# Performance work log

Measured on AMD Instinct MI355X. Metric: run time of the kernel, lower is better.

The kernel has to match this reference:

```python
import jax, jax.numpy as jnp
import numpy as np
import math

MODULE_NUM = 256
OUTPUT_DIM = 257
HID = 64          # self.hidden_dim
STEP_DIM = 16
BATCH = 1024
SOS = MODULE_NUM + 1
EOS = MODULE_NUM
MAX_LEN = MODULE_NUM


def setup_inputs() -> dict:
    key = jax.random.key(0)
    ks = jax.random.split(key, 12)
    s = 0.05
    f32 = jnp.float32
    return {
        "step": 100,
        "batch_size": BATCH,
        "token_embed": jax.random.normal(ks[0], (MODULE_NUM + 2, HID), f32) * s,
        "step_table": jax.random.normal(ks[1], (MAX_LEN + 1, STEP_DIM), f32) * s,
        "w_ih_f": jax.random.normal(ks[2], (3 * HID, HID), f32) * s,
        "w_hh_f": jax.random.normal(ks[3], (3 * HID, HID), f32) * s,
        "b_ih_f": jax.random.normal(ks[4], (3 * HID,), f32) * s,
        "b_hh_f": jax.random.normal(ks[5], (3 * HID,), f32) * s,
        "w_ih_b": jax.random.normal(ks[6], (3 * HID, HID), f32) * s,
        "w_hh_b": jax.random.normal(ks[7], (3 * HID, HID), f32) * s,
        "b_ih_b": jax.random.normal(ks[8], (3 * HID,), f32) * s,
        "b_hh_b": jax.random.normal(ks[9], (3 * HID,), f32) * s,
        "film_w": jax.random.normal(ks[10], (4 * HID, STEP_DIM), f32) * s,
        "film_b": jnp.zeros((4 * HID,), f32),
        "dec_w": jax.random.normal(ks[11], (OUTPUT_DIM, 2 * HID), f32) * s,
        "dec_b": jnp.zeros((OUTPUT_DIM,), f32),
    }


def _gru_cell(x, h, w_ih, w_hh, b_ih, b_hh):
    # PyTorch GRU cell math
    gi = x @ w_ih.T + b_ih              # [B, 3H]
    gh = h @ w_hh.T + b_hh              # [B, 3H]
    i_r, i_z, i_n = jnp.split(gi, 3, axis=-1)
    h_r, h_z, h_n = jnp.split(gh, 3, axis=-1)
    r = jax.nn.sigmoid(i_r + h_r)
    z = jax.nn.sigmoid(i_z + h_z)
    n = jnp.tanh(i_n + r * h_n)
    return (1.0 - z) * n + z * h


def reference(step, batch_size, token_embed, step_table,
              w_ih_f, w_hh_f, b_ih_f, b_hh_f,
              w_ih_b, w_hh_b, b_ih_b, b_hh_b,
              film_w, film_b, dec_w, dec_b):
    # exponential-decay temperature (host scalar, matches _exp_decay_tau)
    tau_max, tau_min, half_life = 2.5, 0.2, 3000
    decay = math.log(2.0) / max(1, half_life)
    temperature = max(1e-06, tau_min + (tau_max - tau_min) * math.exp(-decay * max(0, int(step))))
    B = int(batch_size)

    def step_fn(carry, t):
        h_f, h_b, inp, sel, done = carry
        x = token_embed[inp]                              # [B, H]
        h_f2 = _gru_cell(x, h_f, w_ih_f, w_hh_f, b_ih_f, b_hh_f)
        h_b2 = _gru_cell(x, h_b, w_ih_b, w_hh_b, b_ih_b, b_hh_b)
        hs = jnp.concatenate([h_f2, h_b2], axis=-1)       # [B, 2H]
        film = jnp.tanh(step_table[t] @ film_w.T + film_b)  # [4H]
        gamma, beta = jnp.split(film, 2)
        hs = hs * (1.0 + gamma) + beta
        logits = hs @ dec_w.T + dec_b                     # [B, V]
        masked = jnp.where(sel, -jnp.inf, logits) / temperature
        logp = jax.nn.log_softmax(masked, axis=-1)
        action = jnp.argmax(logp, axis=-1)                # greedy (is_val=True)
        lp = jnp.take_along_axis(logp, action[:, None], axis=-1)[:, 0]
        valid = ~done
        done2 = done | (action == EOS)
        sel2 = sel.at[jnp.arange(B), action].set(True)
        return (h_f2, h_b2, action.astype(jnp.int32), sel2, done2), (action.astype(jnp.int32), lp * valid, valid)

    init = (jnp.zeros((B, HID), jnp.float32),
            jnp.zeros((B, HID), jnp.float32),
            jnp.full((B,), SOS, jnp.int32),
            jnp.zeros((B, OUTPUT_DIM), bool),
            jnp.zeros((B,), bool))
    _, (actions, log_probs, valid) = jax.lax.scan(step_fn, init, jnp.arange(MAX_LEN))
    # [B, L] layout; positions after EOS are masked out via `valid`
    return actions.T, log_probs.T, valid.T
```

## Files before the change

kernel.cpp:

```cpp
#include <hip/hip_runtime.h>
#include <cmath>

typedef float v2f __attribute__((ext_vector_type(2)));

#define GI_STRIDE (258*192)
#define FILM_OFF  (2*GI_STRIDE)
#define TOTAL_PRE (FILM_OFF + 256*256)

#define B_TOT   1024
#define L_MAX   256
#define SOS_TOK 257
#define EOS_TOK 256

#define KEEPF(x) asm volatile("" : "+v"(x))

#define PK_LO(acc, w, x) asm("v_pk_fma_f32 %0, %1, %2, %0 op_sel:[0,0,0] op_sel_hi:[1,0,1]" : "+v"(acc) : "v"(w), "v"(x))
#define PK_HI(acc, w, x) asm("v_pk_fma_f32 %0, %1, %2, %0 op_sel:[0,1,0] op_sel_hi:[1,1,1]" : "+v"(acc) : "v"(w), "v"(x))

#define DPPI(old, src, ctrl, rmask) __builtin_amdgcn_update_dpp(old, src, ctrl, rmask, 0xF, false)

#define AMAX_STAGE(ctrl, rmask) do { \
    const int   _vi = __builtin_bit_cast(int, mv); \
    const float _ov = __builtin_bit_cast(float, DPPI(_vi, _vi, ctrl, rmask)); \
    const int   _oi = DPPI(mi, mi, ctrl, rmask); \
    if (_ov > mv || (_ov == mv && _oi < mi)) { mv = _ov; mi = _oi; } \
} while (0)

#define SUM_STAGE(s, ctrl, rmask) do { \
    (s) += __builtin_bit_cast(float, DPPI(0, __builtin_bit_cast(int, (s)), ctrl, rmask)); \
} while (0)

#define AMAX64() do { \
    AMAX_STAGE(0x111, 0xF); AMAX_STAGE(0x112, 0xF); \
    AMAX_STAGE(0x114, 0xF); AMAX_STAGE(0x118, 0xF); \
    AMAX_STAGE(0x142, 0xA); AMAX_STAGE(0x143, 0xC); \
} while (0)
#define SUM64(s) do { \
    SUM_STAGE(s, 0x111, 0xF); SUM_STAGE(s, 0x112, 0xF); \
    SUM_STAGE(s, 0x114, 0xF); SUM_STAGE(s, 0x118, 0xF); \
    SUM_STAGE(s, 0x142, 0xA); SUM_STAGE(s, 0x143, 0xC); \
} while (0)
#define SUM16(s) do { \
    SUM_STAGE(s, 0x111, 0xF); SUM_STAGE(s, 0x112, 0xF); \
    SUM_STAGE(s, 0x114, 0xF); SUM_STAGE(s, 0x118, 0xF); \
} while (0)

__global__ __launch_bounds__(256) void aag_precompute(
    const float* __restrict__ token_embed,
    const float* __restrict__ step_table,
    const float* __restrict__ w_ih_f, const float* __restrict__ b_ih_f,
    const float* __restrict__ w_ih_b, const float* __restrict__ b_ih_b,
    const float* __restrict__ film_w, const float* __restrict__ film_b,
    float* __restrict__ ws)
{
    int idx = blockIdx.x * 256 + threadIdx.x;
    if (idx < FILM_OFF) {
        int m     = idx / GI_STRIDE;
        int rem   = idx - m * GI_STRIDE;
        int token = rem / 192;
        int r     = rem - token * 192;
        const float* wih = (m ? w_ih_b : w_ih_f) + r * 64;
        const float* te  = token_embed + token * 64;
        float acc = (m ? b_ih_b : b_ih_f)[r];
        #pragma unroll 8
        for (int k = 0; k < 64; ++k) acc += te[k] * wih[k];
        ws[idx] = acc;
    } else if (idx < TOTAL_PRE) {
        int q  = idx - FILM_OFF;
        int tt = q >> 8, j = q & 255;
        const float* st = step_table + tt * 16;
        const float* fw = film_w + j * 16;
        float acc = film_b[j];
        #pragma unroll
        for (int s = 0; s < 16; ++s) acc += st[s] * fw[s];
        int pos = (j < 128) ? (2 * j) : (2 * (j - 128) + 1);
        ws[FILM_OFF + tt * 256 + pos] = tanhf(acc);
    }
}

__global__ __launch_bounds__(512)
__attribute__((amdgpu_waves_per_eu(2, 2)))
void aag_decode(
    const int* __restrict__ step_ptr,
    const float* __restrict__ w_hh_f, const float* __restrict__ b_hh_f,
    const float* __restrict__ w_hh_b, const float* __restrict__ b_hh_b,
    const float* __restrict__ dec_w, const float* __restrict__ dec_b,
    const float* __restrict__ ws,
    float* __restrict__ out)
{
    __shared__ __align__(16) float hbuf[2][4][64];
    __shared__ __align__(16) float ghL[2][4][192];
    __shared__ __align__(16) float hsL[4][128];
    __shared__ __align__(16) float plL[2][4][264];

    const int tid = threadIdx.x;
    const int wv  = tid >> 6;
    const int ln  = tid & 63;
    const int e   = wv >> 1;
    const int m   = wv & 1;

    float invT;
    {
        int step = step_ptr[0];
        if (step < 0) step = 0;
        double T = 0.2 + 2.3 * exp(-(0.6931471805599453 / 3000.0) * (double)step);
        if (T < 1e-6) T = 1e-6;
        invT = (float)(1.0 / T);
    }

    const bool isDec = (tid < 256);
    const bool isEos = (tid >= 256 && tid < 272);
    const bool isGru = (tid >= 320);
    const int  dh    = tid >> 7;
    const int  dq    = tid & 127;
    const int  gj    = tid - 320;
    const int  gm    = (gj >= 96) ? 1 : 0;
    const int  gp    = gj - 96 * gm;
    const int  ec    = tid - 256;

    v2f wreg[64];
    #pragma unroll
    for (int j = 0; j < 64; ++j) wreg[j] = (v2f){0.f, 0.f};
    v2f bias2 = {0.f, 0.f};
    if (isDec) {
        const float* dw = dec_w + (2 * dq) * 128 + dh * 64;
        #pragma unroll
        for (int k = 0; k < 64; ++k) wreg[k] = (v2f){dw[k], dw[128 + k]};
    } else if (isGru) {
        const float* whh = (gm ? w_hh_b : w_hh_f) + (2 * gp) * 64;
        #pragma unroll
        for (int k = 0; k < 64; ++k) wreg[k] = (v2f){whh[k], whh[64 + k]};
        const float* bhh = (gm ? b_hh_b : b_hh_f) + 2 * gp;
        bias2 = (v2f){bhh[0], bhh[1]};
    } else if (isEos) {
        const float* p = dec_w + 256 * 128 + ec * 8;
        #pragma unroll
        for (int k = 0; k < 4; ++k) wreg[k] = (v2f){p[2 * k], p[2 * k + 1]};
    }
    #pragma unroll
    for (int j = 0; j < 64; ++j) KEEPF(wreg[j]);
    KEEPF(bias2);

    float db0 = dec_b[ln], db1 = dec_b[64 + ln];
    float db2 = dec_b[128 + ln], db3 = dec_b[192 + ln];
    float db4 = (ln == 0) ? dec_b[256] : 0.f;
    KEEPF(db0); KEEPF(db1); KEEPF(db2); KEEPF(db3); KEEPF(db4);

    ((float*)hbuf)[tid] = 0.f;
    if (isGru) {
        #pragma unroll
        for (int e2 = 0; e2 < 4; ++e2)
            *(v2f*)&ghL[gm][e2][2 * gp] = bias2;
    }

    bool s0m = false, s1m = false, s2m = false, s3m = false, s4m = false;
    bool done = false;

    const float* filmT = ws + FILM_OFF;
    const float* giT   = ws + m * GI_STRIDE;
    float ga, be;
    {
        const float2 f = *(const float2*)&filmT[(m * 64 + ln) * 2];
        ga = f.x; be = f.y;
    }
    float gi_r, gi_z, gi_n;
    {
        const float* gp2 = giT + SOS_TOK * 192;
        gi_r = gp2[ln]; gi_z = gp2[64 + ln]; gi_n = gp2[128 + ln];
    }

    const int b0 = blockIdx.x * 4;
    float* __restrict__ out_act = out;
    float* __restrict__ out_lp  = out + B_TOT * L_MAX;
    float* __restrict__ out_val = out + 2 * B_TOT * L_MAX;

    __syncthreads();

    for (int t = 0; t <= L_MAX; ++t) {
        if (t > 0) {
            const float u0 = plL[0][e][ln]       + plL[1][e][ln]       + db0;
            const float u1 = plL[0][e][64 + ln]  + plL[1][e][64 + ln]  + db1;
            const float u2 = plL[0][e][128 + ln] + plL[1][e][128 + ln] + db2;
            const float u3 = plL[0][e][192 + ln] + plL[1][e][192 + ln] + db3;
            float mv = s0m ? -INFINITY : u0;
            int   mi = ln;
            { const float v = s1m ? -INFINITY : u1; if (v > mv) { mv = v; mi = 64 + ln; } }
            { const float v = s2m ? -INFINITY : u2; if (v > mv) { mv = v; mi = 128 + ln; } }
            { const float v = s3m ? -INFINITY : u3; if (v > mv) { mv = v; mi = 192 + ln; } }
            float u4 = 0.f;
            if (ln == 0) {
                u4 = plL[0][e][256] + db4;
                const float v = s4m ? -INFINITY : u4;
                if (v > mv) { mv = v; mi = 256; }
            }
            AMAX64();
            const int   a   = __builtin_amdgcn_readlane(mi, 63);
            const float mvU = __builtin_bit_cast(float,
                                __builtin_amdgcn_readlane(__builtin_bit_cast(int, mv), 63));
            {
                const float* gp2 = giT + a * 192;
                gi_r = gp2[ln]; gi_z = gp2[64 + ln]; gi_n = gp2[128 + ln];
            }
            float S = 0.f;
            if (!s0m) S += __expf((u0 - mvU) * invT);
            if (!s1m) S += __expf((u1 - mvU) * invT);
            if (!s2m) S += __expf((u2 - mvU) * invT);
            if (!s3m) S += __expf((u3 - mvU) * invT);
            if (ln == 0 && !s4m) S += __expf((u4 - mvU) * invT);
            SUM64(S);
            const float Su = __builtin_bit_cast(float,
                                __builtin_amdgcn_readlane(__builtin_bit_cast(int, S), 63));
            const bool wasdone = done;
            if (a == EOS_TOK) done = true;
            if ((a & 63) == ln) {
                if (a < 64) s0m = true; else if (a < 128) s1m = true;
                else if (a < 192) s2m = true; else if (a < 256) s3m = true;
                else s4m = true;
            }
            if (ln == 0 && m == 0) {
                const int b = b0 + e;
                out_act[b * L_MAX + (t - 1)] = (float)a;
                out_lp [b * L_MAX + (t - 1)] = wasdone ? 0.f : -__logf(Su);
                out_val[b * L_MAX + (t - 1)] = wasdone ? 0.f : 1.f;
            }
        }
        if (t == L_MAX) break;

        {
            const float hr = ghL[m][e][ln];
            const float hz = ghL[m][e][64 + ln];
            const float hn = ghL[m][e][128 + ln];
            const float hp = hbuf[m][e][ln];
            const float r  = 1.f / (1.f + expf(-(gi_r + hr)));
            const float z  = 1.f / (1.f + expf(-(gi_z + hz)));
            const float n  = tanhf(gi_n + r * hn);
            const float h2 = (1.f - z) * n + z * hp;
            hbuf[m][e][ln] = h2;
            hsL[e][m * 64 + ln] = h2 * (1.f + ga) + be;
        }
        __syncthreads();

        {
            const int tn = (t + 1 < L_MAX) ? t + 1 : L_MAX - 1;
            const float2 f = *(const float2*)&filmT[tn * 256 + (m * 64 + ln) * 2];
            ga = f.x; be = f.y;
        }
        if (isDec) {
            v2f a0 = {0,0}, a1 = {0,0}, a2 = {0,0}, a3 = {0,0};
            const int hb = dh * 64;
            #pragma unroll
            for (int jj = 0; jj < 16; ++jj) {
                const float4 x0 = *(const float4*)&hsL[0][hb + 4 * jj];
                const float4 x1 = *(const float4*)&hsL[1][hb + 4 * jj];
                const float4 x2 = *(const float4*)&hsL[2][hb + 4 * jj];
                const float4 x3 = *(const float4*)&hsL[3][hb + 4 * jj];
                const v2f w0 = wreg[4*jj], w1 = wreg[4*jj+1], w2 = wreg[4*jj+2], w3 = wreg[4*jj+3];
                v2f p;
                p = (v2f){x0.x, x0.y}; PK_LO(a0, w0, p); PK_HI(a0, w1, p);
                p = (v2f){x0.z, x0.w}; PK_LO(a0, w2, p); PK_HI(a0, w3, p);
                p = (v2f){x1.x, x1.y}; PK_LO(a1, w0, p); PK_HI(a1, w1, p);
                p = (v2f){x1.z, x1.w}; PK_LO(a1, w2, p); PK_HI(a1, w3, p);
                p = (v2f){x2.x, x2.y}; PK_LO(a2, w0, p); PK_HI(a2, w1, p);
                p = (v2f){x2.z, x2.w}; PK_LO(a2, w2, p); PK_HI(a2, w3, p);
                p = (v2f){x3.x, x3.y}; PK_LO(a3, w0, p); PK_HI(a3, w1, p);
                p = (v2f){x3.z, x3.w}; PK_LO(a3, w2, p); PK_HI(a3, w3, p);
            }
            *(v2f*)&plL[dh][0][2 * dq] = a0;
            *(v2f*)&plL[dh][1][2 * dq] = a1;
            *(v2f*)&plL[dh][2][2 * dq] = a2;
            *(v2f*)&plL[dh][3][2 * dq] = a3;
        } else if (isGru) {
            v2f a0 = bias2, a1 = bias2, a2 = bias2, a3 = bias2;
            #pragma unroll
            for (int jj = 0; jj < 16; ++jj) {
                const float4 x0 = *(const float4*)&hbuf[gm][0][4 * jj];
                const float4 x1 = *(const float4*)&hbuf[gm][1][4 * jj];
                const float4 x2 = *(const float4*)&hbuf[gm][2][4 * jj];
                const float4 x3 = *(const float4*)&hbuf[gm][3][4 * jj];
                const v2f w0 = wreg[4*jj], w1 = wreg[4*jj+1], w2 = wreg[4*jj+2], w3 = wreg[4*jj+3];
                v2f p;
                p = (v2f){x0.x, x0.y}; PK_LO(a0, w0, p); PK_HI(a0, w1, p);
                p = (v2f){x0.z, x0.w}; PK_LO(a0, w2, p); PK_HI(a0, w3, p);
                p = (v2f){x1.x, x1.y}; PK_LO(a1, w0, p); PK_HI(a1, w1, p);
                p = (v2f){x1.z, x1.w}; PK_LO(a1, w2, p); PK_HI(a1, w3, p);
                p = (v2f){x2.x, x2.y}; PK_LO(a2, w0, p); PK_HI(a2, w1, p);
                p = (v2f){x2.z, x2.w}; PK_LO(a2, w2, p); PK_HI(a2, w3, p);
                p = (v2f){x3.x, x3.y}; PK_LO(a3, w0, p); PK_HI(a3, w1, p);
                p = (v2f){x3.z, x3.w}; PK_LO(a3, w2, p); PK_HI(a3, w3, p);
            }
            *(v2f*)&ghL[gm][0][2 * gp] = a0;
            *(v2f*)&ghL[gm][1][2 * gp] = a1;
            *(v2f*)&ghL[gm][2][2 * gp] = a2;
            *(v2f*)&ghL[gm][3][2 * gp] = a3;
        } else if (isEos) {
            float t0, t1, t2, t3;
            {
                const float4 p0 = *(const float4*)&hsL[0][8 * ec];
                const float4 p1 = *(const float4*)&hsL[0][8 * ec + 4];
                t0 = p0.x*wreg[0].x + p0.y*wreg[0].y + p0.z*wreg[1].x + p0.w*wreg[1].y
                   + p1.x*wreg[2].x + p1.y*wreg[2].y + p1.z*wreg[3].x + p1.w*wreg[3].y;
            }
            {
                const float4 p0 = *(const float4*)&hsL[1][8 * ec];
                const float4 p1 = *(const float4*)&hsL[1][8 * ec + 4];
                t1 = p0.x*wreg[0].x + p0.y*wreg[0].y + p0.z*wreg[1].x + p0.w*wreg[1].y
                   + p1.x*wreg[2].x + p1.y*wreg[2].y + p1.z*wreg[3].x + p1.w*wreg[3].y;
            }
            {
                const float4 p0 = *(const float4*)&hsL[2][8 * ec];
                const float4 p1 = *(const float4*)&hsL[2][8 * ec + 4];
                t2 = p0.x*wreg[0].x + p0.y*wreg[0].y + p0.z*wreg[1].x + p0.w*wreg[1].y
                   + p1.x*wreg[2].x + p1.y*wreg[2].y + p1.z*wreg[3].x + p1.w*wreg[3].y;
            }
            {
                const float4 p0 = *(const float4*)&hsL[3][8 * ec];
                const float4 p1 = *(const float4*)&hsL[3][8 * ec + 4];
                t3 = p0.x*wreg[0].x + p0.y*wreg[0].y + p0.z*wreg[1].x + p0.w*wreg[1].y
                   + p1.x*wreg[2].x + p1.y*wreg[2].y + p1.z*wreg[3].x + p1.w*wreg[3].y;
            }
            SUM16(t0); SUM16(t1); SUM16(t2); SUM16(t3);
            if (ec == 15) {
                plL[0][0][256] = t0; plL[0][1][256] = t1;
                plL[0][2][256] = t2; plL[0][3][256] = t3;
                plL[1][0][256] = 0.f; plL[1][1][256] = 0.f;
                plL[1][2][256] = 0.f; plL[1][3][256] = 0.f;
            }
        }
        __syncthreads();
    }
}

extern "C" void kernel_launch(void* const* d_in, const int* in_sizes, int n_in,
                              void* d_out, int out_size, void* d_ws, size_t ws_size,
                              hipStream_t stream)
{
    const int*   step        = (const int*)  d_in[0];
    const float* token_embed = (const float*)d_in[2];
    const float* step_table  = (const float*)d_in[3];
    const float* w_ih_f = (const float*)d_in[4];
    const float* w_hh_f = (const float*)d_in[5];
    const float* b_ih_f = (const float*)d_in[6];
    const float* b_hh_f = (const float*)d_in[7];
    const float* w_ih_b = (const float*)d_in[8];
    const float* w_hh_b = (const float*)d_in[9];
    const float* b_ih_b = (const float*)d_in[10];
    const float* b_hh_b = (const float*)d_in[11];
    const float* film_w = (const float*)d_in[12];
    const float* film_b = (const float*)d_in[13];
    const float* dec_w  = (const float*)d_in[14];
    const float* dec_b  = (const float*)d_in[15];
    float* ws   = (float*)d_ws;
    float* outp = (float*)d_out;

    aag_precompute<<<TOTAL_PRE / 256, 256, 0, stream>>>(
        token_embed, step_table, w_ih_f, b_ih_f, w_ih_b, b_ih_b,
        film_w, film_b, ws);
    aag_decode<<<256, 512, 0, stream>>>(
        step, w_hh_f, b_hh_f, w_hh_b, b_hh_b, dec_w, dec_b, ws, outp);
}
```

Before: 694.0 us.

## Split batch into two groups and ping-pong softmax/GRU with matvec phases

Splits each block's four batch rows into two groups of two and runs two phases per timestep. In each phase, one group's waves do the argmax/softmax and GRU update while the decoder/GRU matvec waves compute on the other group's data. The aim is to overlap the serial softmax/GRU tail with the matvec work that previously waited behind a barrier. In exchange it doubles the number of barriers per step and halves the batch amortization per matvec pass. It also drops the zero-writes to plL[1][*][256], which relies on those entries being zeroed once at setup.

Measured after the change: 1.117 ms. 1.61x slower.

```diff
diff --git a/kernel.cpp b/kernel.cpp
--- a/kernel.cpp
+++ b/kernel.cpp
@@ -176,31 +176,98 @@
 
     __syncthreads();
 
-    for (int t = 0; t <= L_MAX; ++t) {
-        if (t > 0) {
-            const float u0 = plL[0][e][ln]       + plL[1][e][ln]       + db0;
-            const float u1 = plL[0][e][64 + ln]  + plL[1][e][64 + ln]  + db1;
-            const float u2 = plL[0][e][128 + ln] + plL[1][e][128 + ln] + db2;
-            const float u3 = plL[0][e][192 + ln] + plL[1][e][192 + ln] + db3;
+    auto phase = [&](int k, int g, int eb, bool doDecP, bool doGruP) {
+        const bool mySM = ((wv >> 2) == g);
+        const bool doSM = mySM && (k > 0);
+        const bool doG  = mySM && (k < L_MAX);
+
+        float u0 = 0.f, u1 = 0.f, u2 = 0.f, u3 = 0.f, u4 = 0.f, mvU = 0.f;
+        int a = 0;
+        if (doSM) {
+            u0 = plL[0][e][ln]       + plL[1][e][ln]       + db0;
+            u1 = plL[0][e][64 + ln]  + plL[1][e][64 + ln]  + db1;
+            u2 = plL[0][e][128 + ln] + plL[1][e][128 + ln] + db2;
+            u3 = plL[0][e][192 + ln] + plL[1][e][192 + ln] + db3;
             float mv = s0m ? -INFINITY : u0;
             int   mi = ln;
             { const float v = s1m ? -INFINITY : u1; if (v > mv) { mv = v; mi = 64 + ln; } }
             { const float v = s2m ? -INFINITY : u2; if (v > mv) { mv = v; mi = 128 + ln; } }
             { const float v = s3m ? -INFINITY : u3; if (v > mv) { mv = v; mi = 192 + ln; } }
-            float u4 = 0.f;
             if (ln == 0) {
                 u4 = plL[0][e][256] + db4;
                 const float v = s4m ? -INFINITY : u4;
                 if (v > mv) { mv = v; mi = 256; }
             }
             AMAX64();
-            const int   a   = __builtin_amdgcn_readlane(mi, 63);
-            const float mvU = __builtin_bit_cast(float,
-                                __builtin_amdgcn_readlane(__builtin_bit_cast(int, mv), 63));
+            a   = __builtin_amdgcn_readlane(mi, 63);
+            mvU = __builtin_bit_cast(float,
+                    __builtin_amdgcn_readlane(__builtin_bit_cast(int, mv), 63));
+            const float* gp2 = giT + a * 192;
+            gi_r = gp2[ln]; gi_z = gp2[64 + ln]; gi_n = gp2[128 + ln];
+        }
+        float hr = 0.f, hz = 0.f, hn = 0.f, hp = 0.f;
+        if (doG) {
+            hr = ghL[m][e][ln];
+            hz = ghL[m][e][64 + ln];
+            hn = ghL[m][e][128 + ln];
+            hp = hbuf[m][e][ln];
+        }
+
+        if (doDecP && isDec) {
+            v2f a0 = {0, 0}, a1 = {0, 0};
+            const int hb = dh * 64;
+            #pragma unroll
+            for (int jj = 0; jj < 16; ++jj) {
+                const float4 x0 = *(const float4*)&hsL[eb][hb + 4 * jj];
+                const float4 x1 = *(const float4*)&hsL[eb + 1][hb + 4 * jj];
+                const v2f w0 = wreg[4*jj], w1 = wreg[4*jj+1], w2 = wreg[4*jj+2], w3 = wreg[4*jj+3];
+                v2f p;
+                p = (v2f){x0.x, x0.y}; PK_LO(a0, w0, p); PK_HI(a0, w1, p);
+                p = (v2f){x0.z, x0.w}; PK_LO(a0, w2, p); PK_HI(a0, w3, p);
+                p = (v2f){x1.x, x1.y}; PK_LO(a1, w0, p); PK_HI(a1, w1, p);
+                p = (v2f){x1.z, x1.w}; PK_LO(a1, w2, p); PK_HI(a1, w3, p);
+            }
+            *(v2f*)&plL[dh][eb][2 * dq]     = a0;
+            *(v2f*)&plL[dh][eb + 1][2 * dq] = a1;
+        }
+        if (doGruP && isGru) {
+            v2f a0 = bias2, a1 = bias2;
+            #pragma unroll
+            for (int jj = 0; jj < 16; ++jj) {
+                const float4 x0 = *(const float4*)&hbuf[gm][eb][4 * jj];
+                const float4 x1 = *(const float4*)&hbuf[gm][eb + 1][4 * jj];
+                const v2f w0 = wreg[4*jj], w1 = wreg[4*jj+1], w2 = wreg[4*jj+2], w3 = wreg[4*jj+3];
+                v2f p;
+                p = (v2f){x0.x, x0.y}; PK_LO(a0, w0, p); PK_HI(a0, w1, p);
+                p = (v2f){x0.z, x0.w}; PK_LO(a0, w2, p); PK_HI(a0, w3, p);
+                p = (v2f){x1.x, x1.y}; PK_LO(a1, w0, p); PK_HI(a1, w1, p);
+                p = (v2f){x1.z, x1.w}; PK_LO(a1, w2, p); PK_HI(a1, w3, p);
+            }
+            *(v2f*)&ghL[gm][eb][2 * gp]     = a0;
+            *(v2f*)&ghL[gm][eb + 1][2 * gp] = a1;
+        }
+        if (doDecP && isEos) {
+            float t0, t1;
             {
-                const float* gp2 = giT + a * 192;
-                gi_r = gp2[ln]; gi_z = gp2[64 + ln]; gi_n = gp2[128 + ln];
-            }
+                const float4 p0 = *(const float4*)&hsL[eb][8 * ec];
+                const float4 p1 = *(const float4*)&hsL[eb][8 * ec + 4];
+                t0 = p0.x*wreg[0].x + p0.y*wreg[0].y + p0.z*wreg[1].x + p0.w*wreg[1].y
+                   + p1.x*wreg[2].x + p1.y*wreg[2].y + p1.z*wreg[3].x + p1.w*wreg[3].y;
+            }
+            {
+                const float4 p0 = *(const float4*)&hsL[eb + 1][8 * ec];
+                const float4 p1 = *(const float4*)&hsL[eb + 1][8 * ec + 4];
+                t1 = p0.x*wreg[0].x + p0.y*wreg[0].y + p0.z*wreg[1].x + p0.w*wreg[1].y
+                   + p1.x*wreg[2].x + p1.y*wreg[2].y + p1.z*wreg[3].x + p1.w*wreg[3].y;
+            }
+            SUM16(t0); SUM16(t1);
+            if (ec == 15) {
+                plL[0][eb][256]     = t0;
+                plL[0][eb + 1][256] = t1;
+            }
+        }
+
+        if (doSM) {
             float S = 0.f;
             if (!s0m) S += __expf((u0 - mvU) * invT);
             if (!s1m) S += __expf((u1 - mvU) * invT);
@@ -219,113 +286,29 @@
             }
             if (ln == 0 && m == 0) {
                 const int b = b0 + e;
-                out_act[b * L_MAX + (t - 1)] = (float)a;
-                out_lp [b * L_MAX + (t - 1)] = wasdone ? 0.f : -__logf(Su);
-                out_val[b * L_MAX + (t - 1)] = wasdone ? 0.f : 1.f;
-            }
-        }
-        if (t == L_MAX) break;
-
-        {
-            const float hr = ghL[m][e][ln];
-            const float hz = ghL[m][e][64 + ln];
-            const float hn = ghL[m][e][128 + ln];
-            const float hp = hbuf[m][e][ln];
+                out_act[b * L_MAX + (k - 1)] = (float)a;
+                out_lp [b * L_MAX + (k - 1)] = wasdone ? 0.f : -__logf(Su);
+                out_val[b * L_MAX + (k - 1)] = wasdone ? 0.f : 1.f;
+            }
+        }
+
+        if (doG) {
             const float r  = 1.f / (1.f + expf(-(gi_r + hr)));
             const float z  = 1.f / (1.f + expf(-(gi_z + hz)));
             const float n  = tanhf(gi_n + r * hn);
             const float h2 = (1.f - z) * n + z * hp;
             hbuf[m][e][ln] = h2;
             hsL[e][m * 64 + ln] = h2 * (1.f + ga) + be;
-        }
-        __syncthreads();
-
-        {
-            const int tn = (t + 1 < L_MAX) ? t + 1 : L_MAX - 1;
+            const int tn = (k + 1 < L_MAX) ? k + 1 : L_MAX - 1;
             const float2 f = *(const float2*)&filmT[tn * 256 + (m * 64 + ln) * 2];
             ga = f.x; be = f.y;
         }
-        if (isDec) {
-            v2f a0 = {0,0}, a1 = {0,0}, a2 = {0,0}, a3 = {0,0};
-            const int hb = dh * 64;
-            #pragma unroll
-            for (int jj = 0; jj < 16; ++jj) {
-                const float4 x0 = *(const float4*)&hsL[0][hb + 4 * jj];
-                const float4 x1 = *(const float4*)&hsL[1][hb + 4 * jj];
-                const float4 x2 = *(const float4*)&hsL[2][hb + 4 * jj];
-                const float4 x3 = *(const float4*)&hsL[3][hb + 4 * jj];
-                const v2f w0 = wreg[4*jj], w1 = wreg[4*jj+1], w2 = wreg[4*jj+2], w3 = wreg[4*jj+3];
-                v2f p;
-                p = (v2f){x0.x, x0.y}; PK_LO(a0, w0, p); PK_HI(a0, w1, p);
-                p = (v2f){x0.z, x0.w}; PK_LO(a0, w2, p); PK_HI(a0, w3, p);
-                p = (v2f){x1.x, x1.y}; PK_LO(a1, w0, p); PK_HI(a1, w1, p);
-                p = (v2f){x1.z, x1.w}; PK_LO(a1, w2, p); PK_HI(a1, w3, p);
-                p = (v2f){x2.x, x2.y}; PK_LO(a2, w0, p); PK_HI(a2, w1, p);
-                p = (v2f){x2.z, x2.w}; PK_LO(a2, w2, p); PK_HI(a2, w3, p);
-                p = (v2f){x3.x, x3.y}; PK_LO(a3, w0, p); PK_HI(a3, w1, p);
-                p = (v2f){x3.z, x3.w}; PK_LO(a3, w2, p); PK_HI(a3, w3, p);
-            }
-            *(v2f*)&plL[dh][0][2 * dq] = a0;
-            *(v2f*)&plL[dh][1][2 * dq] = a1;
-            *(v2f*)&plL[dh][2][2 * dq] = a2;
-            *(v2f*)&plL[dh][3][2 * dq] = a3;
-        } else if (isGru) {
-            v2f a0 = bias2, a1 = bias2, a2 = bias2, a3 = bias2;
-            #pragma unroll
-            for (int jj = 0; jj < 16; ++jj) {
-                const float4 x0 = *(const float4*)&hbuf[gm][0][4 * jj];
-                const float4 x1 = *(const float4*)&hbuf[gm][1][4 * jj];
-                const float4 x2 = *(const float4*)&hbuf[gm][2][4 * jj];
-                const float4 x3 = *(const float4*)&hbuf[gm][3][4 * jj];
-                const v2f w0 = wreg[4*jj], w1 = wreg[4*jj+1], w2 = wreg[4*jj+2], w3 = wreg[4*jj+3];
-                v2f p;
-                p = (v2f){x0.x, x0.y}; PK_LO(a0, w0, p); PK_HI(a0, w1, p);
-                p = (v2f){x0.z, x0.w}; PK_LO(a0, w2, p); PK_HI(a0, w3, p);
-                p = (v2f){x1.x, x1.y}; PK_LO(a1, w0, p); PK_HI(a1, w1, p);
-                p = (v2f){x1.z, x1.w}; PK_LO(a1, w2, p); PK_HI(a1, w3, p);
-                p = (v2f){x2.x, x2.y}; PK_LO(a2, w0, p); PK_HI(a2, w1, p);
-                p = (v2f){x2.z, x2.w}; PK_LO(a2, w2, p); PK_HI(a2, w3, p);
-                p = (v2f){x3.x, x3.y}; PK_LO(a3, w0, p); PK_HI(a3, w1, p);
-                p = (v2f){x3.z, x3.w}; PK_LO(a3, w2, p); PK_HI(a3, w3, p);
-            }
-            *(v2f*)&ghL[gm][0][2 * gp] = a0;
-            *(v2f*)&ghL[gm][1][2 * gp] = a1;
-            *(v2f*)&ghL[gm][2][2 * gp] = a2;
-            *(v2f*)&ghL[gm][3][2 * gp] = a3;
-        } else if (isEos) {
-            float t0, t1, t2, t3;
-            {
-                const float4 p0 = *(const float4*)&hsL[0][8 * ec];
-                const float4 p1 = *(const float4*)&hsL[0][8 * ec + 4];
-                t0 = p0.x*wreg[0].x + p0.y*wreg[0].y + p0.z*wreg[1].x + p0.w*wreg[1].y
-                   + p1.x*wreg[2].x + p1.y*wreg[2].y + p1.z*wreg[3].x + p1.w*wreg[3].y;
-            }
-            {
-                const float4 p0 = *(const float4*)&hsL[1][8 * ec];
-                const float4 p1 = *(const float4*)&hsL[1][8 * ec + 4];
-                t1 = p0.x*wreg[0].x + p0.y*wreg[0].y + p0.z*wreg[1].x + p0.w*wreg[1].y
-                   + p1.x*wreg[2].x + p1.y*wreg[2].y + p1.z*wreg[3].x + p1.w*wreg[3].y;
-            }
-            {
-                const float4 p0 = *(const float4*)&hsL[2][8 * ec];
-                const float4 p1 = *(const float4*)&hsL[2][8 * ec + 4];
-                t2 = p0.x*wreg[0].x + p0.y*wreg[0].y + p0.z*wreg[1].x + p0.w*wreg[1].y
-                   + p1.x*wreg[2].x + p1.y*wreg[2].y + p1.z*wreg[3].x + p1.w*wreg[3].y;
-            }
-            {
-                const float4 p0 = *(const float4*)&hsL[3][8 * ec];
-                const float4 p1 = *(const float4*)&hsL[3][8 * ec + 4];
-                t3 = p0.x*wreg[0].x + p0.y*wreg[0].y + p0.z*wreg[1].x + p0.w*wreg[1].y
-                   + p1.x*wreg[2].x + p1.y*wreg[2].y + p1.z*wreg[3].x + p1.w*wreg[3].y;
-            }
-            SUM16(t0); SUM16(t1); SUM16(t2); SUM16(t3);
-            if (ec == 15) {
-                plL[0][0][256] = t0; plL[0][1][256] = t1;
-                plL[0][2][256] = t2; plL[0][3][256] = t3;
-                plL[1][0][256] = 0.f; plL[1][1][256] = 0.f;
-                plL[1][2][256] = 0.f; plL[1][3][256] = 0.f;
-            }
-        }
+    };
+
+    for (int k = 0; k <= L_MAX; ++k) {
+        phase(k, 0, 2, k > 0, (k >= 1) && (k < L_MAX));
+        __syncthreads();
+        phase(k, 1, 0, k < L_MAX, k < L_MAX - 1);
         __syncthreads();
     }
 }
```
